# Performance work log

Measured on AMD Instinct MI355X. Metric: run time of the kernel, lower is better.

Reference implementation:

```python
import jax, jax.numpy as jnp
import numpy as np
import math

B, H, S, F = 2, 16, 2048, 128

def setup_inputs() -> dict:
    key = jax.random.key(0)
    ks = jax.random.split(key, 7)
    scale = 1.0 / math.sqrt(F)
    x = jax.random.normal(ks[0], (B, H, S, F), dtype=jnp.float32)
    # torch nn.Linear weight is [out, in]; stacked per head -> [H, out, in]
    Wq = jax.random.uniform(ks[1], (H, F, F), jnp.float32, -scale, scale)
    Wk = jax.random.uniform(ks[2], (H, F, F), jnp.float32, -scale, scale)
    Wv = jax.random.uniform(ks[3], (H, F, F), jnp.float32, -scale, scale)
    bq = jax.random.uniform(ks[4], (H, F), jnp.float32, -scale, scale)
    bk = jax.random.uniform(ks[5], (H, F), jnp.float32, -scale, scale)
    bv = jax.random.uniform(ks[6], (H, F), jnp.float32, -scale, scale)
    return {"x": x, "Wq": Wq, "Wk": Wk, "Wv": Wv, "bq": bq, "bk": bk, "bv": bv}

def reference(x, Wq, Wk, Wv, bq, bk, bv):
    # Per-head linear projections (y = x @ W.T + b), batched over heads via einsum
    q = jnp.einsum('bhsf,hef->bhse', x, Wq) + bq[None, :, None, :]
    k = jnp.einsum('bhsf,hef->bhse', x, Wk) + bk[None, :, None, :]
    v = jnp.einsum('bhsf,hef->bhse', x, Wv) + bv[None, :, None, :]
    # Scores [B,H,S,S]
    scores = jnp.einsum('bhqe,bhke->bhqk', q, k)
    # Causal mask (strict upper triangle set to -inf) applied BEFORE scaling,
    # matching the original (dividing -inf by sqrt(F) keeps it -inf)
    causal = jnp.triu(jnp.ones((S, S), dtype=bool), k=1)
    scores = jnp.where(causal[None, None], -jnp.inf, scores)
    scores = scores / jnp.sqrt(jnp.float32(x.shape[-1]))
    weights = jax.nn.softmax(scores, axis=-1)
    return jnp.einsum('bhqk,bhke->bhqe', weights, v)
```

## Files before the change

kernel.cpp:

```cpp
#include <hip/hip_runtime.h>
#include <hip/hip_bf16.h>

#define SLEN 2048
#define FDIM 128
#define NH   16
#define NBH  32
#define QBLK 64
#define KVB  64
#define NQT  (SLEN / QBLK)

typedef __attribute__((ext_vector_type(8)))  __bf16 bf16x8;
typedef __attribute__((ext_vector_type(8)))  short  s16x8;
typedef __attribute__((ext_vector_type(4)))  short  s16x4;
typedef __attribute__((ext_vector_type(4)))  float  f32x4;
typedef __attribute__((ext_vector_type(16))) float  f32x16;
typedef __attribute__((ext_vector_type(4)))  int    i32x4;

__device__ __forceinline__ unsigned short f2bf_u(float f) {
    union { float f; unsigned u; } t;
    t.f = f;
    unsigned r = t.u + 0x7FFFu + ((t.u >> 16) & 1u);
    return (unsigned short)(r >> 16);
}
__device__ __forceinline__ short f2bf(float f) { return (short)f2bf_u(f); }

__device__ __forceinline__ unsigned cvt_pk_bf16(float lo, float hi) {
    unsigned r;
    asm("v_cvt_pk_bf16_f32 %0, %1, %2" : "=v"(r) : "v"(lo), "v"(hi));
    return r;
}

__device__ __forceinline__ float ex2(float x) {
    float r;
    asm volatile("v_exp_f32 %0, %1" : "=v"(r) : "v"(x));
    return r;
}

__device__ __forceinline__ void gld16(const void* g, void* l) {
    __builtin_amdgcn_global_load_lds(
        (const __attribute__((address_space(1))) void*)g,
        (__attribute__((address_space(3))) void*)l, 16, 0, 0);
}

__global__ __launch_bounds__(256, 4) void wconv(
    const float* __restrict__ Wq, const float* __restrict__ Wk,
    const float* __restrict__ Wv, short* __restrict__ Wb)
{
    const int bid = blockIdx.x;
    const int z = bid >> 6, rem = bid & 63;
    const int h = rem >> 2, qd = rem & 3;
    const float* Wm = ((z == 0) ? Wq : (z == 1) ? Wk : Wv) + (size_t)h * 16384;
    short* O = Wb + ((size_t)z * NH + h) * 16384;
    const int t = threadIdx.x;
    #pragma unroll
    for (int it = 0; it < 2; ++it) {
        int idx = qd * 4096 + it * 2048 + t * 8;
        int e = idx >> 7, c = idx & 127;
        f32x4 a = *(const f32x4*)&Wm[idx];
        f32x4 b = *(const f32x4*)&Wm[idx + 4];
        union { unsigned u[4]; s16x8 v; } o;
        o.u[0] = cvt_pk_bf16(a[0], a[1]);
        o.u[1] = cvt_pk_bf16(a[2], a[3]);
        o.u[2] = cvt_pk_bf16(b[0], b[1]);
        o.u[3] = cvt_pk_bf16(b[2], b[3]);
        *(s16x8*)&O[(e << 7) | (c ^ ((e & 15) << 3))] = o.v;
    }
}

__global__ __launch_bounds__(256, 2) void qkv_fused(
    const float* __restrict__ x, const short* __restrict__ Wb,
    const float* __restrict__ bq, const float* __restrict__ bk, const float* __restrict__ bv,
    short* __restrict__ Q, short* __restrict__ K, short* __restrict__ Vt)
{
    const int bh = blockIdx.y;
    const int h  = bh & (NH - 1);
    const int st = blockIdx.x;
    const float* xg = x + ((size_t)bh * SLEN + st * 64) * FDIM;

    __shared__ __align__(16) short lx[64][136];
    __shared__ __align__(16) short lw[128][128];

    const int t = threadIdx.x;
    const int wid = t >> 6, lane = t & 63;

    #define WSTAGE(zz) do {                                                     \
        const char* wsrc_ = (const char*)(Wb + ((size_t)(zz) * NH + h) * 16384);\
        _Pragma("unroll")                                                       \
        for (int i_ = 0; i_ < 8; ++i_)                                          \
            gld16(wsrc_ + wid * 8192 + i_ * 1024 + lane * 16,                   \
                  (char*)&lw[0][0] + wid * 8192 + i_ * 1024);                   \
    } while (0)

    WSTAGE(0);
    {
        int r = t >> 4, c = (t & 15) * 8;
        #pragma unroll
        for (int it = 0; it < 4; ++it) {
            const float* src = &xg[(size_t)(r + it * 16) * FDIM + c];
            f32x4 a = *(const f32x4*)&src[0];
            f32x4 b = *(const f32x4*)&src[4];
            union { unsigned u[4]; s16x8 v; } o;
            o.u[0] = cvt_pk_bf16(a[0], a[1]);
            o.u[1] = cvt_pk_bf16(a[2], a[3]);
            o.u[2] = cvt_pk_bf16(b[0], b[1]);
            o.u[3] = cvt_pk_bf16(b[2], b[3]);
            *(s16x8*)&lx[r + it * 16][c] = o.v;
        }
    }
    __syncthreads();

    const int wr = (wid >> 1) * 32;
    const int wc = (wid & 1) * 64;
    const int lr = lane & 15, lk = (lane >> 4) * 8, hi4 = (lane >> 4) * 4;
    const short* lwp = &lw[0][0];
    const int swz = lr << 3;

    #pragma unroll
    for (int z = 0; z < 3; ++z) {
        f32x4 acc[2][4] = {};
        #pragma unroll
        for (int ks = 0; ks < 4; ++ks) {
            int kb = ks * 32 + lk;
            bf16x8 a[2], b[4];
            #pragma unroll
            for (int m = 0; m < 2; ++m) a[m] = *(const bf16x8*)&lx[wr + m * 16 + lr][kb];
            #pragma unroll
            for (int n = 0; n < 4; ++n)
                b[n] = *(const bf16x8*)&lwp[(size_t)(wc + n * 16 + lr) * 128 + (kb ^ swz)];
            #pragma unroll
            for (int m = 0; m < 2; ++m)
                #pragma unroll
                for (int n = 0; n < 4; ++n)
                    acc[m][n] = __builtin_amdgcn_mfma_f32_16x16x32_bf16(a[m], b[n], acc[m][n], 0, 0, 0);
        }
        if (z < 2) { __syncthreads(); WSTAGE(z + 1); }

        const float* bias = ((z == 0) ? bq : (z == 1) ? bk : bv) + h * FDIM;
        if (z == 0) {
            short* og = Q + ((size_t)bh * SLEN + st * 64) * FDIM;
            const float sc = 0.12751744526f;
            #pragma unroll
            for (int n = 0; n < 4; ++n) {
                int col = wc + n * 16 + lr;
                float bb = bias[col];
                #pragma unroll
                for (int m = 0; m < 2; ++m) {
                    int r0 = wr + m * 16 + hi4;
                    #pragma unroll
                    for (int j = 0; j < 4; ++j)
                        og[(size_t)(r0 + j) * FDIM + col] = f2bf((acc[m][n][j] + bb) * sc);
                }
            }
        } else if (z == 1) {
            short* og = K + (size_t)bh * SLEN * FDIM;
            #pragma unroll
            for (int n = 0; n < 4; ++n) {
                int col = wc + n * 16 + lr;
                float bb = bias[col];
                #pragma unroll
                for (int m = 0; m < 2; ++m) {
                    int s0 = st * 64 + wr + m * 16 + hi4;
                    #pragma unroll
                    for (int j = 0; j < 4; ++j) {
                        int s = s0 + j;
                        int idx = (s * FDIM + col) ^ ((s & 15) << 3);
                        og[idx] = f2bf(acc[m][n][j] + bb);
                    }
                }
            }
        } else {
            short* ogT = Vt + (size_t)bh * SLEN * FDIM;
            const int hp = (hi4 == 4) ? 8 : (hi4 == 8) ? 4 : hi4;
            #pragma unroll
            for (int n = 0; n < 4; ++n) {
                int col = wc + n * 16 + lr;
                float bb = bias[col];
                const int cb  = col >> 5, qlp = col & 31;
                #pragma unroll
                for (int m = 0; m < 2; ++m) {
                    const int kb16 = wr + m * 16;
                    const int hs_  = kb16 >> 5;
                    const int s2_  = (kb16 >> 4) & 1;
                    const int hi2_ = hp >> 3;
                    const int j0   = hp & 7;
                    union { unsigned u[2]; s16x4 v; } w;
                    w.u[0] = cvt_pk_bf16(acc[m][n][0] + bb, acc[m][n][1] + bb);
                    w.u[1] = cvt_pk_bf16(acc[m][n][2] + bb, acc[m][n][3] + bb);
                    size_t addr = (size_t)st * 8192 + hs_ * 4096 + cb * 1024
                                + s2_ * 512 + (hi2_ * 32 + qlp) * 8 + j0;
                    *(s16x4*)&ogT[addr] = w.v;
                }
            }
        }
        if (z < 2) __syncthreads();
    }
    #undef WSTAGE
}

__global__ __launch_bounds__(256, 2) void attn_fwd(
    const short* __restrict__ Qg, const short* __restrict__ Kg,
    const short* __restrict__ vTg, float* __restrict__ out)
{
    __shared__ __align__(16) char smem[34816];
    float* obuf = (float*)smem;
    float* mlb  = (float*)(smem + 33792);

    const int bid = blockIdx.x;
    const int bh  = bid & 31;
    const int i   = ((bid >> 5) & 7) + ((bid >> 8) << 3);
    const int grp = i >> 3, k = i & 7;
    const int qt  = (grp == 0) ? (31 - k) : (grp == 1) ? (8 + k)
                  : (grp == 2) ? (23 - k) : k;

    const int t = threadIdx.x, wid = t >> 6, lane = t & 63;
    const int ql  = lane & 31;
    const int hi2 = lane >> 5;
    const int qb  = wid & 1;
    const int hs  = wid >> 1;
    const size_t base = (size_t)bh * SLEN * FDIM;

    const char*  kgb = (const char*)(Kg + base);
    const short* vgb = vTg + base + hs * 4096 + (size_t)lane * 8;

    bf16x8 qf[8];
    {
        const short* qp = Qg + base + (size_t)(qt * QBLK + qb * 32 + ql) * FDIM;
        #pragma unroll
        for (int ks = 0; ks < 8; ++ks) qf[ks] = *(const bf16x8*)&qp[ks * 16 + hi2 * 8];
    }

    f32x16 oacc[4] = {};
    float m_run = -1e30f, l_run = 0.f;

    #define STAGE(ktile, buf) do {                                               \
        const char* kt_ = kgb + (size_t)(ktile) * 16384;                         \
        _Pragma("unroll")                                                        \
        for (int i_ = 0; i_ < 4; ++i_)                                           \
            gld16(kt_ + wid * 4096 + i_ * 1024 + lane * 16,                      \
                  smem + (buf) * 16384 + wid * 4096 + i_ * 1024);                \
    } while (0)

    STAGE(0, 0);
    __syncthreads();

    const int nkt = qt + 1;
    int cur = 0;
    const int kswz = (ql & 15) << 3;

    for (int kt = 0; kt < nkt; ++kt) {
        bf16x8 vfr[8];
        {
            const short* vb_ = vgb + (size_t)kt * 8192;
            #pragma unroll
            for (int cb = 0; cb < 4; ++cb) {
                vfr[cb * 2 + 0] = *(const bf16x8*)&vb_[cb * 1024];
                vfr[cb * 2 + 1] = *(const bf16x8*)&vb_[cb * 1024 + 512];
            }
        }
        if (kt + 1 < nkt) STAGE(kt + 1, cur ^ 1);

        const char* kbuf = smem + cur * 16384;

        const int Rrow = hs * 32 + ql;
        f32x16 sfr = {};
        __builtin_amdgcn_s_setprio(1);
        #pragma unroll
        for (int ks = 0; ks < 8; ++ks) {
            bf16x8 kf = *(const bf16x8*)(kbuf + (size_t)(((Rrow * 128 + ks * 16 + hi2 * 8) ^ kswz) * 2));
            sfr = __builtin_amdgcn_mfma_f32_32x32x16_bf16(kf, qf[ks], sfr, 0, 0, 0);
        }
        __builtin_amdgcn_s_setprio(0);

        if (kt == qt) {
            if (hs > qb) {
                #pragma unroll
                for (int r = 0; r < 16; ++r) sfr[r] = -__builtin_inff();
            } else if (hs == qb) {
                #pragma unroll
                for (int r = 0; r < 16; ++r) {
                    int kl = (r & 3) + 8 * (r >> 2) + 4 * hi2;
                    if (kl > ql) sfr[r] = -__builtin_inff();
                }
            }
        }

        float a0 = fmaxf(fmaxf(sfr[0],  sfr[1]),  sfr[2]);
        float a1 = fmaxf(fmaxf(sfr[3],  sfr[4]),  sfr[5]);
        float a2 = fmaxf(fmaxf(sfr[6],  sfr[7]),  sfr[8]);
        float a3 = fmaxf(fmaxf(sfr[9],  sfr[10]), sfr[11]);
        float a4 = fmaxf(fmaxf(sfr[12], sfr[13]), sfr[14]);
        float b0 = fmaxf(fmaxf(a0, a1), a2);
        float b1 = fmaxf(fmaxf(a3, a4), sfr[15]);
        float rm = fmaxf(b0, b1);
        rm = fmaxf(rm, __shfl_xor(rm, 32));
        if (!__all(rm <= m_run + 8.f)) {
            float mnew = fmaxf(m_run, rm);
            float fac  = ex2(m_run - mnew);
            l_run *= fac;
            #pragma unroll
            for (int cb = 0; cb < 4; ++cb) oacc[cb] *= fac;
            m_run = mnew;
        }
        float pe[16];
        #pragma unroll
        for (int r = 0; r < 16; ++r) pe[r] = ex2(sfr[r] - m_run);
        float s0 = (pe[0] + pe[1]) + (pe[2] + pe[3]);
        float s1 = (pe[4] + pe[5]) + (pe[6] + pe[7]);
        float s2 = (pe[8] + pe[9]) + (pe[10] + pe[11]);
        float s3 = (pe[12] + pe[13]) + (pe[14] + pe[15]);
        float ssum = (s0 + s1) + (s2 + s3);
        l_run += ssum + __shfl_xor(ssum, 32);

        bf16x8 pf[2];
        #pragma unroll
        for (int s2_ = 0; s2_ < 2; ++s2_) {
            const int b = s2_ * 8;
            union { unsigned u[4]; bf16x8 v; } w;
            w.u[0] = cvt_pk_bf16(pe[b + 0], pe[b + 1]);
            w.u[1] = cvt_pk_bf16(pe[b + 2], pe[b + 3]);
            w.u[2] = cvt_pk_bf16(pe[b + 4], pe[b + 5]);
            w.u[3] = cvt_pk_bf16(pe[b + 6], pe[b + 7]);
            pf[s2_] = w.v;
        }

        __builtin_amdgcn_s_setprio(1);
        #pragma unroll
        for (int cb = 0; cb < 4; ++cb) {
            #pragma unroll
            for (int s2_ = 0; s2_ < 2; ++s2_)
                oacc[cb] = __builtin_amdgcn_mfma_f32_32x32x16_bf16(vfr[cb * 2 + s2_], pf[s2_], oacc[cb], 0, 0, 0);
        }
        __builtin_amdgcn_s_setprio(0);

        __syncthreads();
        cur ^= 1;
    }
    #undef STAGE

    if (lane < 32) {
        mlb[(wid * 32 + ql) * 2 + 0] = m_run;
        mlb[(wid * 32 + ql) * 2 + 1] = l_run;
    }
    if (hs == 1) {
        #pragma unroll
        for (int cb = 0; cb < 4; ++cb)
            #pragma unroll
            for (int r = 0; r < 16; ++r) {
                int e = cb * 32 + (r & 3) + 8 * (r >> 2) + 4 * hi2;
                obuf[(qb * 32 + ql) * 132 + e] = oacc[cb][r];
            }
    }
    __syncthreads();
    if (hs == 0) {
        float m2 = mlb[((wid + 2) * 32 + ql) * 2 + 0];
        float l2 = mlb[((wid + 2) * 32 + ql) * 2 + 1];
        float M  = fmaxf(m_run, m2);
        float a  = ex2(m_run - M);
        float b2 = ex2(m2 - M);
        float inv = 1.f / (l_run * a + l2 * b2);
        float* orow = out + base + (size_t)(qt * QBLK + qb * 32 + ql) * FDIM;
        #pragma unroll
        for (int cb = 0; cb < 4; ++cb)
            #pragma unroll
            for (int r = 0; r < 16; ++r) {
                int e = cb * 32 + (r & 3) + 8 * (r >> 2) + 4 * hi2;
                orow[e] = (oacc[cb][r] * a + obuf[(qb * 32 + ql) * 132 + e] * b2) * inv;
            }
    }
}

extern "C" void kernel_launch(void* const* d_in, const int* in_sizes, int n_in,
                              void* d_out, int out_size, void* d_ws, size_t ws_size,
                              hipStream_t stream) {
    (void)in_sizes; (void)n_in; (void)out_size;
    const float* x  = (const float*)d_in[0];
    const float* Wq = (const float*)d_in[1];
    const float* Wk = (const float*)d_in[2];
    const float* Wv = (const float*)d_in[3];
    const float* bq = (const float*)d_in[4];
    const float* bk = (const float*)d_in[5];
    const float* bv = (const float*)d_in[6];

    const size_t elems = (size_t)NBH * SLEN * FDIM;
    const size_t wb_shorts = (size_t)3 * NH * FDIM * FDIM;
    short* Q  = (short*)d_ws;
    short* K  = Q + elems;
    short* Vt = K + elems;
    short* Wb = (ws_size >= (3 * elems + wb_shorts) * sizeof(short))
              ? (Vt + elems) : (short*)d_out;

    wconv<<<dim3(192), 256, 0, stream>>>(Wq, Wk, Wv, Wb);
    qkv_fused<<<dim3(SLEN / 64, NBH), 256, 0, stream>>>(x, Wb, bq, bk, bv, Q, K, Vt);
    attn_fwd<<<dim3(NQT * NBH), 256, 0, stream>>>(Q, K, Vt, (float*)d_out);
}
```

Before: 81.35 us.

## Give each wave its own 32-query row and stream K directly from global

The attention kernel now launches 128-thread blocks where each wave owns one 32-row query strip and walks all causal 32-key slices itself. This removes the two-way key split across waves, the LDS double-buffered K staging, per-tile barriers and the final cross-wave softmax merge through shared memory. K fragments are now read straight from global (swizzled layout) and the causal mask only touches the diagonal slice, which skips the fully masked half-tile. In exchange there is no LDS reuse of K across waves, so global/L2 traffic for K and V grows. Each wave's loop is also twice as long and serial, and the setprio hints are dropped.

```diff
diff --git a/kernel.cpp b/kernel.cpp
--- a/kernel.cpp
+++ b/kernel.cpp
@@ -6,7 +6,6 @@
 #define NH   16
 #define NBH  32
 #define QBLK 64
-#define KVB  64
 #define NQT  (SLEN / QBLK)
 
 typedef __attribute__((ext_vector_type(8)))  __bf16 bf16x8;
@@ -14,7 +13,6 @@
 typedef __attribute__((ext_vector_type(4)))  short  s16x4;
 typedef __attribute__((ext_vector_type(4)))  float  f32x4;
 typedef __attribute__((ext_vector_type(16))) float  f32x16;
-typedef __attribute__((ext_vector_type(4)))  int    i32x4;
 
 __device__ __forceinline__ unsigned short f2bf_u(float f) {
     union { float f; unsigned u; } t;
@@ -197,30 +195,25 @@
     #undef WSTAGE
 }
 
-__global__ __launch_bounds__(256, 2) void attn_fwd(
+__global__ __launch_bounds__(128, 4) void attn_fwd(
     const short* __restrict__ Qg, const short* __restrict__ Kg,
     const short* __restrict__ vTg, float* __restrict__ out)
 {
-    __shared__ __align__(16) char smem[34816];
-    float* obuf = (float*)smem;
-    float* mlb  = (float*)(smem + 33792);
-
     const int bid = blockIdx.x;
     const int bh  = bid & 31;
-    const int i   = ((bid >> 5) & 7) + ((bid >> 8) << 3);
-    const int grp = i >> 3, k = i & 7;
-    const int qt  = (grp == 0) ? (31 - k) : (grp == 1) ? (8 + k)
-                  : (grp == 2) ? (23 - k) : k;
-
-    const int t = threadIdx.x, wid = t >> 6, lane = t & 63;
+    const int t = threadIdx.x, wv = t >> 6, lane = t & 63;
     const int ql  = lane & 31;
     const int hi2 = lane >> 5;
-    const int qb  = wid & 1;
-    const int hs  = wid >> 1;
+
+    const int j  = (bid >> 5) & 7;
+    const int w8 = (bid >> 8) * 2 + wv;
+    const int mm = 7 - w8;
+    const int v  = (mm & 1) ? ((mm + 1) * 8 - 1 - j) : (mm * 8 + j);
+    const int qt = v >> 1, qb = v & 1;
+
     const size_t base = (size_t)bh * SLEN * FDIM;
-
     const char*  kgb = (const char*)(Kg + base);
-    const short* vgb = vTg + base + hs * 4096 + (size_t)lane * 8;
+    const short* vgb = vTg + base + (size_t)lane * 8;
 
     bf16x8 qf[8];
     {
@@ -231,56 +224,32 @@
 
     f32x16 oacc[4] = {};
     float m_run = -1e30f, l_run = 0.f;
-
-    #define STAGE(ktile, buf) do {                                               \
-        const char* kt_ = kgb + (size_t)(ktile) * 16384;                         \
-        _Pragma("unroll")                                                        \
-        for (int i_ = 0; i_ < 4; ++i_)                                           \
-            gld16(kt_ + wid * 4096 + i_ * 1024 + lane * 16,                      \
-                  smem + (buf) * 16384 + wid * 4096 + i_ * 1024);                \
-    } while (0)
-
-    STAGE(0, 0);
-    __syncthreads();
-
-    const int nkt = qt + 1;
-    int cur = 0;
+    const int nsl = 2 * qt + qb + 1;
     const int kswz = (ql & 15) << 3;
 
-    for (int kt = 0; kt < nkt; ++kt) {
+    for (int sl = 0; sl < nsl; ++sl) {
+        const char*  kt_ = kgb + (size_t)sl * 8192;
+        const short* vb_ = vgb + (size_t)sl * 4096;
+
         bf16x8 vfr[8];
-        {
-            const short* vb_ = vgb + (size_t)kt * 8192;
-            #pragma unroll
-            for (int cb = 0; cb < 4; ++cb) {
-                vfr[cb * 2 + 0] = *(const bf16x8*)&vb_[cb * 1024];
-                vfr[cb * 2 + 1] = *(const bf16x8*)&vb_[cb * 1024 + 512];
-            }
-        }
-        if (kt + 1 < nkt) STAGE(kt + 1, cur ^ 1);
-
-        const char* kbuf = smem + cur * 16384;
-
-        const int Rrow = hs * 32 + ql;
+        #pragma unroll
+        for (int cb = 0; cb < 4; ++cb) {
+            vfr[cb * 2 + 0] = *(const bf16x8*)&vb_[cb * 1024];
+            vfr[cb * 2 + 1] = *(const bf16x8*)&vb_[cb * 1024 + 512];
+        }
+
         f32x16 sfr = {};
-        __builtin_amdgcn_s_setprio(1);
         #pragma unroll
         for (int ks = 0; ks < 8; ++ks) {
-            bf16x8 kf = *(const bf16x8*)(kbuf + (size_t)(((Rrow * 128 + ks * 16 + hi2 * 8) ^ kswz) * 2));
+            bf16x8 kf = *(const bf16x8*)(kt_ + (size_t)(((ql * 128 + ks * 16 + hi2 * 8) ^ kswz) * 2));
             sfr = __builtin_amdgcn_mfma_f32_32x32x16_bf16(kf, qf[ks], sfr, 0, 0, 0);
         }
-        __builtin_amdgcn_s_setprio(0);
-
-        if (kt == qt) {
-            if (hs > qb) {
-                #pragma unroll
-                for (int r = 0; r < 16; ++r) sfr[r] = -__builtin_inff();
-            } else if (hs == qb) {
-                #pragma unroll
-                for (int r = 0; r < 16; ++r) {
-                    int kl = (r & 3) + 8 * (r >> 2) + 4 * hi2;
-                    if (kl > ql) sfr[r] = -__builtin_inff();
-                }
+
+        if (sl == nsl - 1) {
+            #pragma unroll
+            for (int r = 0; r < 16; ++r) {
+                int kl = (r & 3) + 8 * (r >> 2) + 4 * hi2;
+                if (kl > ql) sfr[r] = -__builtin_inff();
             }
         }
 
@@ -323,50 +292,23 @@
             pf[s2_] = w.v;
         }
 
-        __builtin_amdgcn_s_setprio(1);
         #pragma unroll
         for (int cb = 0; cb < 4; ++cb) {
             #pragma unroll
             for (int s2_ = 0; s2_ < 2; ++s2_)
                 oacc[cb] = __builtin_amdgcn_mfma_f32_32x32x16_bf16(vfr[cb * 2 + s2_], pf[s2_], oacc[cb], 0, 0, 0);
         }
-        __builtin_amdgcn_s_setprio(0);
-
-        __syncthreads();
-        cur ^= 1;
-    }
-    #undef STAGE
-
-    if (lane < 32) {
-        mlb[(wid * 32 + ql) * 2 + 0] = m_run;
-        mlb[(wid * 32 + ql) * 2 + 1] = l_run;
-    }
-    if (hs == 1) {
-        #pragma unroll
-        for (int cb = 0; cb < 4; ++cb)
-            #pragma unroll
-            for (int r = 0; r < 16; ++r) {
-                int e = cb * 32 + (r & 3) + 8 * (r >> 2) + 4 * hi2;
-                obuf[(qb * 32 + ql) * 132 + e] = oacc[cb][r];
-            }
-    }
-    __syncthreads();
-    if (hs == 0) {
-        float m2 = mlb[((wid + 2) * 32 + ql) * 2 + 0];
-        float l2 = mlb[((wid + 2) * 32 + ql) * 2 + 1];
-        float M  = fmaxf(m_run, m2);
-        float a  = ex2(m_run - M);
-        float b2 = ex2(m2 - M);
-        float inv = 1.f / (l_run * a + l2 * b2);
-        float* orow = out + base + (size_t)(qt * QBLK + qb * 32 + ql) * FDIM;
-        #pragma unroll
-        for (int cb = 0; cb < 4; ++cb)
-            #pragma unroll
-            for (int r = 0; r < 16; ++r) {
-                int e = cb * 32 + (r & 3) + 8 * (r >> 2) + 4 * hi2;
-                orow[e] = (oacc[cb][r] * a + obuf[(qb * 32 + ql) * 132 + e] * b2) * inv;
-            }
-    }
+    }
+
+    float inv = 1.f / l_run;
+    float* orow = out + base + (size_t)(qt * QBLK + qb * 32 + ql) * FDIM;
+    #pragma unroll
+    for (int cb = 0; cb < 4; ++cb)
+        #pragma unroll
+        for (int r = 0; r < 16; ++r) {
+            int e = cb * 32 + (r & 3) + 8 * (r >> 2) + 4 * hi2;
+            orow[e] = oacc[cb][r] * inv;
+        }
 }
 
 extern "C" void kernel_launch(void* const* d_in, const int* in_sizes, int n_in,
@@ -391,5 +333,5 @@
 
     wconv<<<dim3(192), 256, 0, stream>>>(Wq, Wk, Wv, Wb);
     qkv_fused<<<dim3(SLEN / 64, NBH), 256, 0, stream>>>(x, Wb, bq, bk, bv, Q, K, Vt);
-    attn_fwd<<<dim3(NQT * NBH), 256, 0, stream>>>(Q, K, Vt, (float*)d_out);
-}
+    attn_fwd<<<dim3(NQT * NBH), 128, 0, stream>>>(Q, K, Vt, (float*)d_out);
+}
```

Result: slower. 263.8 us (+224.3%).
